# Performance work log

Measured on AMD Instinct MI355X. Metric: run time of the kernel, lower is better.

The kernel has to match this reference:

```python
import jax, jax.numpy as jnp
import numpy as np

N = 50000   # nodes
E = 1600000 # edges
K = 5       # Chebyshev order
F_IN, H1, H2, P = 32, 32, 16, 12


def setup_inputs() -> dict:
    key = jax.random.key(0)
    ks = jax.random.split(key, 16)
    x = jax.random.normal(ks[0], (N, F_IN), dtype=jnp.float32)
    edge_index = jax.random.randint(ks[1], (2, E), 0, N, dtype=jnp.int64)
    edge_weight = jax.random.uniform(ks[2], (E,), dtype=jnp.float32)
    s = 0.1
    # Cell 1: 3 gates (z, r, h), each with x-conv [K,F_IN,H1] and h-conv [K,H1,H1]
    Wx1 = jax.random.normal(ks[3], (3, K, F_IN, H1), dtype=jnp.float32) * s
    bx1 = jax.random.normal(ks[4], (3, H1), dtype=jnp.float32) * s
    Wh1 = jax.random.normal(ks[5], (3, K, H1, H1), dtype=jnp.float32) * s
    bh1 = jax.random.normal(ks[6], (3, H1), dtype=jnp.float32) * s
    # Cell 2
    Wx2 = jax.random.normal(ks[7], (3, K, H1, H2), dtype=jnp.float32) * s
    bx2 = jax.random.normal(ks[8], (3, H2), dtype=jnp.float32) * s
    Wh2 = jax.random.normal(ks[9], (3, K, H2, H2), dtype=jnp.float32) * s
    bh2 = jax.random.normal(ks[10], (3, H2), dtype=jnp.float32) * s
    # Output linear (torch convention: weight [out,in])
    Wl = jax.random.normal(ks[11], (P, H2), dtype=jnp.float32) * s
    bl = jax.random.normal(ks[12], (P,), dtype=jnp.float32) * s
    return dict(x=x, edge_index=edge_index, edge_weight=edge_weight,
                Wx1=Wx1, bx1=bx1, Wh1=Wh1, bh1=bh1,
                Wx2=Wx2, bx2=bx2, Wh2=Wh2, bh2=bh2, Wl=Wl, bl=bl)


def _cheb_norm(edge_index, edge_weight):
    # ChebConv 'sym' norm with lambda_max=2: L_hat off-diagonal = -D^-1/2 A D^-1/2,
    # diagonal cancels to 0 (get_laplacian +1 self loop, add_self_loops fill -1).
    row, col = edge_index[0], edge_index[1]
    deg = jax.ops.segment_sum(edge_weight, row, num_segments=N)
    dis = jnp.where(deg > 0, jax.lax.rsqrt(jnp.maximum(deg, 1e-30)), 0.0)
    return -dis[row] * edge_weight * dis[col]


def _gconv_gru_forward(x, edge_index, edge_weight, Wx1, bx1, Wh1, bh1,
                       Wx2, bx2, Wh2, bh2, Wl, bl):
    row, col = edge_index[0], edge_index[1]
    wn = _cheb_norm(edge_index, edge_weight)

    def spmm(v):  # (L_hat @ v): gather source rows, scatter-add to targets
        return jax.ops.segment_sum(v[row] * wn[:, None], col, num_segments=N)

    def cheb(v, W, b):  # W: [K, Fin, Fout]
        Tx0 = v
        out = Tx0 @ W[0]
        Tx1 = spmm(Tx0)
        out = out + Tx1 @ W[1]
        for k in range(2, K):
            Tx2 = 2.0 * spmm(Tx1) - Tx0
            out = out + Tx2 @ W[k]
            Tx0, Tx1 = Tx1, Tx2
        return out + b

    def gru_cell(v, H, Wx, bx, Wh, bh):
        Z = jax.nn.sigmoid(cheb(v, Wx[0], bx[0]) + cheb(H, Wh[0], bh[0]))
        R = jax.nn.sigmoid(cheb(v, Wx[1], bx[1]) + cheb(H, Wh[1], bh[1]))
        Ht = jnp.tanh(cheb(v, Wx[2], bx[2]) + cheb(H * R, Wh[2], bh[2]))
        return Z * H + (1.0 - Z) * Ht

    h = gru_cell(x, jnp.zeros((N, H1), x.dtype), Wx1, bx1, Wh1, bh1)
    h = jax.nn.relu(h)  # dropout is identity in eval mode
    h = gru_cell(h, jnp.zeros((N, H2), x.dtype), Wx2, bx2, Wh2, bh2)
    h = jax.nn.relu(h)
    return h @ Wl.T + bl


def reference(x, edge_index, edge_weight, Wx1, bx1, Wh1, bh1,
              Wx2, bx2, Wh2, bh2, Wl, bl):
    return _gconv_gru_forward(x, edge_index, edge_weight, Wx1, bx1, Wh1, bh1,
                              Wx2, bx2, Wh2, bh2, Wl, bl)
```

## Files before the change

### kernel.cpp

```cpp
#include <hip/hip_runtime.h>
#include <math.h>

#define NN 50000
#define NE 1600000
#define KORD 5
#define NB 196
#define QTR 12500
#define GE 782
#define MT 64
#define NBK 1563
#define NBP 1600
#define NCH 128
#define ECH (NE / NCH)
#define EC4 (NE / 64)
#define PADE 1800192

#define SCALE_W 2097152.0f
#define INV_SCALE_W (1.0f / 2097152.0f)
#define SCALE_D 4194304.0f
#define INV_SCALE_D (1.0f / 4194304.0f)

typedef _Float16 half8 __attribute__((ext_vector_type(8)));
typedef _Float16 half4v __attribute__((ext_vector_type(4)));
typedef float float4v __attribute__((ext_vector_type(4)));

__global__ __launch_bounds__(1024) void k_deg(const int* __restrict__ ei,
                                              const float* __restrict__ ew,
                                              int* __restrict__ deg_g) {
    __shared__ int h[QTR];
    int q = blockIdx.x >> 6, ch = blockIdx.x & 63;
    for (int i = threadIdx.x; i < QTR; i += 1024) h[i] = 0;
    __syncthreads();
    int base = ch * EC4, lo = q * QTR;
    for (int e = base + threadIdx.x; e < base + EC4; e += 1024) {
        int li = ei[e] - lo;
        if ((unsigned)li < (unsigned)QTR)
            atomicAdd(&h[li], __float2int_rn(ew[e] * SCALE_D));
    }
    __syncthreads();
    int* outp = deg_g + blockIdx.x * QTR;
    for (int i = threadIdx.x; i < QTR; i += 1024) outp[i] = h[i];
}

__global__ __launch_bounds__(256) void k_dis2(const int* __restrict__ deg_g,
                                              float* __restrict__ dis) {
    int n = blockIdx.x * 256 + threadIdx.x;
    if (n >= NN) return;
    int q = n / QTR, i = n % QTR;
    const int* p = deg_g + (q * 64) * QTR + i;
    int s = 0;
#pragma unroll
    for (int c = 0; c < 64; c++) s += p[c * QTR];
    float d = (float)s * INV_SCALE_D;
    dis[n] = s > 0 ? rsqrtf(fmaxf(d, 1e-30f)) : 0.f;
}

__global__ __launch_bounds__(1024) void k_bhist(const int* __restrict__ ei,
                                                int* __restrict__ bh) {
    __shared__ int hist[NBK];
    int ch = blockIdx.x;
    for (int i = threadIdx.x; i < NBK; i += 1024) hist[i] = 0;
    __syncthreads();
    const int* cols = ei + NE;
    int base = ch * ECH;
    for (int e = base + threadIdx.x; e < base + ECH; e += 1024)
        atomicAdd(&hist[cols[e] >> 5], 1);
    __syncthreads();
    int* outp = bh + ch * NBP;
    for (int b = threadIdx.x; b < NBK; b += 1024) outp[b] = hist[b];
}

__global__ __launch_bounds__(256) void k_btot(const int* __restrict__ bh,
                                              int* __restrict__ tot) {
    int b = blockIdx.x * 256 + threadIdx.x;
    if (b >= NBP) return;
    int s = 0;
    if (b < NBK) {
#pragma unroll 8
        for (int ch = 0; ch < NCH; ch++) s += bh[ch * NBP + b];
    }
    tot[b] = s;
}

__global__ __launch_bounds__(1024) void k_bscan1(const int* __restrict__ tot,
                                                 int* __restrict__ off_bk) {
    __shared__ int s[1024];
    int t = threadIdx.x;
    int a0 = (2 * t < NBP) ? tot[2 * t] : 0;
    int a1 = (2 * t + 1 < NBP) ? tot[2 * t + 1] : 0;
    int p0 = (a0 + 127) & ~127;
    int p1 = (a1 + 127) & ~127;
    s[t] = p0 + p1;
    __syncthreads();
    for (int d = 1; d < 1024; d <<= 1) {
        int u = (t >= d) ? s[t - d] : 0;
        __syncthreads();
        s[t] += u;
        __syncthreads();
    }
    int excl = (t == 0) ? 0 : s[t - 1];
    if (2 * t < NBK) off_bk[2 * t] = excl;
    if (2 * t + 1 < NBK) off_bk[2 * t + 1] = excl + p0;
    if (t == 1023) off_bk[NBK] = s[1023];
}

__global__ __launch_bounds__(256) void k_bcur(int* __restrict__ bh,
                                              const int* __restrict__ off_bk) {
    int b = blockIdx.x * 256 + threadIdx.x;
    if (b >= NBK) return;
    int run = off_bk[b];
    for (int ch = 0; ch < NCH; ch++) {
        int v = bh[ch * NBP + b];
        bh[ch * NBP + b] = run;
        run += v;
    }
}

__global__ __launch_bounds__(128) void k_pad(const int* __restrict__ off_bk,
                                             const int* __restrict__ tot,
                                             int2* __restrict__ edges) {
    int b = blockIdx.x;
    int start = off_bk[b] + tot[b];
    int end = off_bk[b + 1];
    for (int i = start + threadIdx.x; i < end; i += 128)
        edges[i] = make_int2(0, 0);
}

__global__ __launch_bounds__(1024) void k_cperm(const int* __restrict__ ei,
                                                const float* __restrict__ ew,
                                                const float* __restrict__ dis,
                                                const int* __restrict__ bh,
                                                int2* __restrict__ edges) {
    __shared__ int cur[NBK];
    int ch = blockIdx.x;
    const int* cp = bh + ch * NBP;
    for (int b = threadIdx.x; b < NBK; b += 1024) cur[b] = cp[b];
    __syncthreads();
    int base = ch * ECH;
    for (int e = base + threadIdx.x; e < base + ECH; e += 1024) {
        int r = ei[e], c = ei[NE + e];
        float w = -dis[r] * ew[e] * dis[c];
        int pos = atomicAdd(&cur[c >> 5], 1);
        int packed = (int)((unsigned)r | ((unsigned)(c & 31) << 16));
        edges[pos] = make_int2(packed, __float_as_int(w));
    }
}

__global__ __launch_bounds__(256) void k_spmm(const int* __restrict__ off_bk,
                                              const int2* __restrict__ edges,
                                              const float* __restrict__ vin,
                                              const float* __restrict__ prev,
                                              float* __restrict__ vout,
                                              float scale) {
    __shared__ int acc[32][33];
    int b = blockIdx.x;
    for (int i = threadIdx.x; i < 32 * 33; i += 256) (&acc[0][0])[i] = 0;
    __syncthreads();
    int e0 = off_bk[b], e1 = off_bk[b + 1];
    int group = threadIdx.x >> 3, sub = threadIdx.x & 7;
    const float4* vin4 = (const float4*)vin;
    int i = e0 + group;
    if (i < e1) {
        int2 ea = edges[i];
        int2 eb = edges[i + 32];
        int2 ec = edges[i + 64];
        int2 ed = edges[i + 96];
        while (true) {
            int ni = i + 128;
            bool more = ni < e1;
            int2 na, nb, nc, nd;
            if (more) {
                na = edges[ni];
                nb = edges[ni + 32];
                nc = edges[ni + 64];
                nd = edges[ni + 96];
            }
            unsigned ra = (unsigned)ea.x, rb = (unsigned)eb.x;
            unsigned rc = (unsigned)ec.x, rd = (unsigned)ed.x;
            float4 va = vin4[(ra & 0xffffu) * 8 + sub];
            float4 vb = vin4[(rb & 0xffffu) * 8 + sub];
            float4 vc = vin4[(rc & 0xffffu) * 8 + sub];
            float4 vd = vin4[(rd & 0xffffu) * 8 + sub];
            float wa = __int_as_float(ea.y) * SCALE_W;
            float wb = __int_as_float(eb.y) * SCALE_W;
            float wc = __int_as_float(ec.y) * SCALE_W;
            float wd = __int_as_float(ed.y) * SCALE_W;
            int* aa = &acc[ra >> 16][sub * 4];
            int* ab = &acc[rb >> 16][sub * 4];
            int* ac = &acc[rc >> 16][sub * 4];
            int* ad = &acc[rd >> 16][sub * 4];
            atomicAdd(aa + 0, __float2int_rn(wa * va.x));
            atomicAdd(aa + 1, __float2int_rn(wa * va.y));
            atomicAdd(aa + 2, __float2int_rn(wa * va.z));
            atomicAdd(aa + 3, __float2int_rn(wa * va.w));
            atomicAdd(ab + 0, __float2int_rn(wb * vb.x));
            atomicAdd(ab + 1, __float2int_rn(wb * vb.y));
            atomicAdd(ab + 2, __float2int_rn(wb * vb.z));
            atomicAdd(ab + 3, __float2int_rn(wb * vb.w));
            atomicAdd(ac + 0, __float2int_rn(wc * vc.x));
            atomicAdd(ac + 1, __float2int_rn(wc * vc.y));
            atomicAdd(ac + 2, __float2int_rn(wc * vc.z));
            atomicAdd(ac + 3, __float2int_rn(wc * vc.w));
            atomicAdd(ad + 0, __float2int_rn(wd * vd.x));
            atomicAdd(ad + 1, __float2int_rn(wd * vd.y));
            atomicAdd(ad + 2, __float2int_rn(wd * vd.z));
            atomicAdd(ad + 3, __float2int_rn(wd * vd.w));
            if (!more) break;
            i = ni; ea = na; eb = nb; ec = nc; ed = nd;
        }
    }
    __syncthreads();
    float sf = scale * INV_SCALE_W;
    int base = b << 5;
    int nl = threadIdx.x >> 3, s4 = threadIdx.x & 7;
    int n = base + nl;
    if (n < NN) {
        const int* a = &acc[nl][s4 * 4];
        float4 o;
        if (prev) {
            float4 p = ((const float4*)prev)[n * 8 + s4];
            o = make_float4(fmaf(sf, (float)a[0], -p.x),
                            fmaf(sf, (float)a[1], -p.y),
                            fmaf(sf, (float)a[2], -p.z),
                            fmaf(sf, (float)a[3], -p.w));
        } else {
            o = make_float4(sf * (float)a[0], sf * (float)a[1],
                            sf * (float)a[2], sf * (float)a[3]);
        }
        ((float4*)vout)[n * 8 + s4] = o;
    }
}

__global__ __launch_bounds__(256) void k_epi1(
    const float* __restrict__ x, const float* __restrict__ t1,
    const float* __restrict__ t2, const float* __restrict__ t3,
    const float* __restrict__ t4, const float* __restrict__ Wx1,
    const float* __restrict__ bx1, const float* __restrict__ bh1,
    float* __restrict__ h) {
    __shared__ _Float16 T[5][MT][40];
    __shared__ _Float16 Wt[64][168];
    int n0 = blockIdx.x * MT;
    const float* bufs[5] = {x, t1, t2, t3, t4};
#pragma unroll
    for (int b = 0; b < 5; b++) {
        for (int idx = threadIdx.x; idx < MT * 8; idx += 256) {
            int r = idx >> 3, c4 = idx & 7;
            int rr = n0 + r; if (rr >= NN) rr = NN - 1;
            float4 v = *(const float4*)(bufs[b] + rr * 32 + c4 * 4);
            *(half4v*)&T[b][r][c4 * 4] =
                (half4v){(_Float16)v.x, (_Float16)v.y, (_Float16)v.z, (_Float16)v.w};
        }
    }
    const float* Wz = Wx1;
    const float* Wh = Wx1 + 2 * KORD * 32 * 32;
    for (int idx = threadIdx.x; idx < 160 * 64; idx += 256) {
        int k = idx >> 6, n = idx & 63;
        int b = k >> 5, i = k & 31;
        float w = (n < 32) ? Wz[b * 1024 + i * 32 + n]
                           : Wh[b * 1024 + i * 32 + (n - 32)];
        Wt[n][k] = (_Float16)w;
    }
    __syncthreads();
    int wave = threadIdx.x >> 6;
    int lane = threadIdx.x & 63;
    int lo = lane & 15, quad = lane >> 4;
    float4v acc[4];
#pragma unroll
    for (int t = 0; t < 4; t++) acc[t] = (float4v){0.f, 0.f, 0.f, 0.f};
#pragma unroll
    for (int b = 0; b < 5; b++) {
        half8 a = *(half8*)&T[b][wave * 16 + lo][quad * 8];
#pragma unroll
        for (int t = 0; t < 4; t++) {
            half8 bf = *(half8*)&Wt[t * 16 + lo][b * 32 + quad * 8];
            acc[t] = __builtin_amdgcn_mfma_f32_16x16x32_f16(a, bf, acc[t], 0, 0, 0);
        }
    }
    int nd_base = n0 + wave * 16 + quad * 4;
#pragma unroll
    for (int t = 0; t < 2; t++) {
        int j = t * 16 + lo;
        float bz = bx1[j] + bh1[j];
        float bhb = bx1[64 + j] + bh1[64 + j];
#pragma unroll
        for (int reg = 0; reg < 4; reg++) {
            int nd = nd_base + reg;
            if (nd < NN) {
                float zz = acc[t][reg] + bz;
                float hh = acc[t + 2][reg] + bhb;
                float z = 1.f / (1.f + __expf(-zz));
                float tt = __expf(-2.f * fabsf(hh));
                float ht = copysignf((1.f - tt) / (1.f + tt), hh);
                h[nd * 32 + j] = fmaxf((1.f - z) * ht, 0.f);
            }
        }
    }
}

__global__ __launch_bounds__(256) void k_epi2(
    const float* __restrict__ hin, const float* __restrict__ t1,
    const float* __restrict__ t2, const float* __restrict__ t3,
    const float* __restrict__ t4, const float* __restrict__ Wx2,
    const float* __restrict__ bx2, const float* __restrict__ bh2,
    const float* __restrict__ Wl, const float* __restrict__ bl,
    float* __restrict__ out) {
    __shared__ _Float16 T[5][MT][40];
    __shared__ _Float16 Wt[32][168];
    __shared__ float H2[MT][17];
    int n0 = blockIdx.x * MT;
    const float* bufs[5] = {hin, t1, t2, t3, t4};
#pragma unroll
    for (int b = 0; b < 5; b++) {
        for (int idx = threadIdx.x; idx < MT * 8; idx += 256) {
            int r = idx >> 3, c4 = idx & 7;
            int rr = n0 + r; if (rr >= NN) rr = NN - 1;
            float4 v = *(const float4*)(bufs[b] + rr * 32 + c4 * 4);
            *(half4v*)&T[b][r][c4 * 4] =
                (half4v){(_Float16)v.x, (_Float16)v.y, (_Float16)v.z, (_Float16)v.w};
        }
    }
    const float* Wz = Wx2;
    const float* Wh = Wx2 + 2 * KORD * 32 * 16;
    for (int idx = threadIdx.x; idx < 160 * 32; idx += 256) {
        int k = idx >> 5, n = idx & 31;
        int b = k >> 5, i = k & 31;
        float w = (n < 16) ? Wz[b * 512 + i * 16 + n]
                           : Wh[b * 512 + i * 16 + (n - 16)];
        Wt[n][k] = (_Float16)w;
    }
    __syncthreads();
    int wave = threadIdx.x >> 6;
    int lane = threadIdx.x & 63;
    int lo = lane & 15, quad = lane >> 4;
    float4v acc[2];
    acc[0] = (float4v){0.f, 0.f, 0.f, 0.f};
    acc[1] = (float4v){0.f, 0.f, 0.f, 0.f};
#pragma unroll
    for (int b = 0; b < 5; b++) {
        half8 a = *(half8*)&T[b][wave * 16 + lo][quad * 8];
#pragma unroll
        for (int t = 0; t < 2; t++) {
            half8 bf = *(half8*)&Wt[t * 16 + lo][b * 32 + quad * 8];
            acc[t] = __builtin_amdgcn_mfma_f32_16x16x32_f16(a, bf, acc[t], 0, 0, 0);
        }
    }
    {
        int j = lo;
        float bz = bx2[j] + bh2[j];
        float bhb = bx2[32 + j] + bh2[32 + j];
        int ndl_base = wave * 16 + quad * 4;
#pragma unroll
        for (int reg = 0; reg < 4; reg++) {
            float zz = acc[0][reg] + bz;
            float hh = acc[1][reg] + bhb;
            float z = 1.f / (1.f + __expf(-zz));
            float tt = __expf(-2.f * fabsf(hh));
            float ht = copysignf((1.f - tt) / (1.f + tt), hh);
            H2[ndl_base + reg][j] = fmaxf((1.f - z) * ht, 0.f);
        }
    }
    __syncthreads();
    for (int idx = threadIdx.x; idx < MT * 12; idx += 256) {
        int n = idx / 12, p = idx % 12;
        int gn = n0 + n;
        if (gn < NN) {
            float o = bl[p];
#pragma unroll
            for (int jj = 0; jj < 16; jj++) o = fmaf(H2[n][jj], Wl[p * 16 + jj], o);
            out[gn * 12 + p] = o;
        }
    }
}


extern "C" void kernel_launch(void* const* d_in, const int* in_sizes, int n_in,
                              void* d_out, int out_size, void* d_ws, size_t ws_size,
                              hipStream_t stream) {
    const float* x   = (const float*)d_in[0];
    const int*   ei  = (const int*)d_in[1];
    const float* ew  = (const float*)d_in[2];
    const float* Wx1 = (const float*)d_in[3];
    const float* bx1 = (const float*)d_in[4];
    const float* bh1 = (const float*)d_in[6];
    const float* Wx2 = (const float*)d_in[7];
    const float* bx2 = (const float*)d_in[8];
    const float* bh2 = (const float*)d_in[10];
    const float* Wl  = (const float*)d_in[11];
    const float* bl  = (const float*)d_in[12];
    float* out = (float*)d_out;

    float* ws     = (float*)d_ws;
    float* dis    = ws;
    int*   bh     = (int*)(ws + 50048);
    int*   tot    = bh + NCH * NBP;
    int*   off_bk = tot + NBP;
    int2*  edges  = (int2*)(off_bk + NBP);
    float* T1     = (float*)(edges + PADE);
    float* T2     = T1 + NN * 32;
    float* T3     = T2 + NN * 32;
    float* T4     = T3 + NN * 32;
    float* hb     = T4 + NN * 32;
    int*   deg_g  = (int*)T1;

    k_deg  <<<256, 1024, 0, stream>>>(ei, ew, deg_g);
    k_dis2 <<<NB, 256, 0, stream>>>(deg_g, dis);
    k_bhist<<<NCH, 1024, 0, stream>>>(ei, bh);
    k_btot <<<7, 256, 0, stream>>>(bh, tot);
    k_bscan1<<<1, 1024, 0, stream>>>(tot, off_bk);
    k_bcur <<<7, 256, 0, stream>>>(bh, off_bk);
    k_pad  <<<NBK, 128, 0, stream>>>(off_bk, tot, edges);
    k_cperm<<<NCH, 1024, 0, stream>>>(ei, ew, dis, bh, edges);

    k_spmm<<<NBK, 256, 0, stream>>>(off_bk, edges, x,  nullptr, T1, 1.f);
    k_spmm<<<NBK, 256, 0, stream>>>(off_bk, edges, T1, x,       T2, 2.f);
    k_spmm<<<NBK, 256, 0, stream>>>(off_bk, edges, T2, T1,      T3, 2.f);
    k_spmm<<<NBK, 256, 0, stream>>>(off_bk, edges, T3, T2,      T4, 2.f);
    k_epi1<<<GE, 256, 0, stream>>>(x, T1, T2, T3, T4, Wx1, bx1, bh1, hb);

    k_spmm<<<NBK, 256, 0, stream>>>(off_bk, edges, hb, nullptr, T1, 1.f);
    k_spmm<<<NBK, 256, 0, stream>>>(off_bk, edges, T1, hb,      T2, 2.f);
    k_spmm<<<NBK, 256, 0, stream>>>(off_bk, edges, T2, T1,      T3, 2.f);
    k_spmm<<<NBK, 256, 0, stream>>>(off_bk, edges, T3, T2,      T4, 2.f);
    k_epi2<<<GE, 256, 0, stream>>>(hb, T1, T2, T3, T4, Wx2, bx2, bh2, Wl, bl, out);
}
```

Baseline: 376.4 us.

## Software-pipeline SpMM gathers one iteration ahead of LDS atomics; double bucketing chunks

The SpMM inner loop now issues the feature-row gathers for the current edge group and then performs the shared-memory atomic accumulation for the previous group's gathered values. This two-stage pipeline is meant to hide global gather latency behind LDS atomics. Separately, NCH doubles from 128 to 256, so the edge-bucketing kernels run with more, smaller chunks and more blocks. The pipeline holds more live registers (an extra set of float4 values), which may lower occupancy.

```diff
diff --git a/kernel.cpp b/kernel.cpp
--- a/kernel.cpp
+++ b/kernel.cpp
@@ -10,7 +10,7 @@
 #define MT 64
 #define NBK 1563
 #define NBP 1600
-#define NCH 128
+#define NCH 256
 #define ECH (NE / NCH)
 #define EC4 (NE / 64)
 #define PADE 1800192
@@ -146,6 +146,30 @@
     }
 }
 
+#define SPMM_DS(C0, W0, G0, C1, W1, G1, C2, W2, G2, C3, W3, G3)      \
+    {                                                                 \
+        int* a0 = &acc[C0][sub * 4];                                  \
+        int* a1 = &acc[C1][sub * 4];                                  \
+        int* a2 = &acc[C2][sub * 4];                                  \
+        int* a3 = &acc[C3][sub * 4];                                  \
+        atomicAdd(a0 + 0, __float2int_rn(W0 * G0.x));                 \
+        atomicAdd(a0 + 1, __float2int_rn(W0 * G0.y));                 \
+        atomicAdd(a0 + 2, __float2int_rn(W0 * G0.z));                 \
+        atomicAdd(a0 + 3, __float2int_rn(W0 * G0.w));                 \
+        atomicAdd(a1 + 0, __float2int_rn(W1 * G1.x));                 \
+        atomicAdd(a1 + 1, __float2int_rn(W1 * G1.y));                 \
+        atomicAdd(a1 + 2, __float2int_rn(W1 * G1.z));                 \
+        atomicAdd(a1 + 3, __float2int_rn(W1 * G1.w));                 \
+        atomicAdd(a2 + 0, __float2int_rn(W2 * G2.x));                 \
+        atomicAdd(a2 + 1, __float2int_rn(W2 * G2.y));                 \
+        atomicAdd(a2 + 2, __float2int_rn(W2 * G2.z));                 \
+        atomicAdd(a2 + 3, __float2int_rn(W2 * G2.w));                 \
+        atomicAdd(a3 + 0, __float2int_rn(W3 * G3.x));                 \
+        atomicAdd(a3 + 1, __float2int_rn(W3 * G3.y));                 \
+        atomicAdd(a3 + 2, __float2int_rn(W3 * G3.z));                 \
+        atomicAdd(a3 + 3, __float2int_rn(W3 * G3.w));                 \
+    }
+
 __global__ __launch_bounds__(256) void k_spmm(const int* __restrict__ off_bk,
                                               const int2* __restrict__ edges,
                                               const float* __restrict__ vin,
@@ -161,53 +185,37 @@
     const float4* vin4 = (const float4*)vin;
     int i = e0 + group;
     if (i < e1) {
-        int2 ea = edges[i];
-        int2 eb = edges[i + 32];
-        int2 ec = edges[i + 64];
-        int2 ed = edges[i + 96];
+        int2 R0 = edges[i], R1 = edges[i + 32], R2 = edges[i + 64], R3 = edges[i + 96];
+        float4 G0, G1, G2, G3;
+        int C0 = 0, C1 = 0, C2 = 0, C3 = 0;
+        float W0 = 0.f, W1 = 0.f, W2 = 0.f, W3 = 0.f;
+        bool haveG = false;
         while (true) {
             int ni = i + 128;
-            bool more = ni < e1;
-            int2 na, nb, nc, nd;
-            if (more) {
-                na = edges[ni];
-                nb = edges[ni + 32];
-                nc = edges[ni + 64];
-                nd = edges[ni + 96];
+            bool moreR = ni < e1;
+            int2 N0, N1, N2, N3;
+            if (moreR) {
+                N0 = edges[ni]; N1 = edges[ni + 32];
+                N2 = edges[ni + 64]; N3 = edges[ni + 96];
             }
-            unsigned ra = (unsigned)ea.x, rb = (unsigned)eb.x;
-            unsigned rc = (unsigned)ec.x, rd = (unsigned)ed.x;
-            float4 va = vin4[(ra & 0xffffu) * 8 + sub];
-            float4 vb = vin4[(rb & 0xffffu) * 8 + sub];
-            float4 vc = vin4[(rc & 0xffffu) * 8 + sub];
-            float4 vd = vin4[(rd & 0xffffu) * 8 + sub];
-            float wa = __int_as_float(ea.y) * SCALE_W;
-            float wb = __int_as_float(eb.y) * SCALE_W;
-            float wc = __int_as_float(ec.y) * SCALE_W;
-            float wd = __int_as_float(ed.y) * SCALE_W;
-            int* aa = &acc[ra >> 16][sub * 4];
-            int* ab = &acc[rb >> 16][sub * 4];
-            int* ac = &acc[rc >> 16][sub * 4];
-            int* ad = &acc[rd >> 16][sub * 4];
-            atomicAdd(aa + 0, __float2int_rn(wa * va.x));
-            atomicAdd(aa + 1, __float2int_rn(wa * va.y));
-            atomicAdd(aa + 2, __float2int_rn(wa * va.z));
-            atomicAdd(aa + 3, __float2int_rn(wa * va.w));
-            atomicAdd(ab + 0, __float2int_rn(wb * vb.x));
-            atomicAdd(ab + 1, __float2int_rn(wb * vb.y));
-            atomicAdd(ab + 2, __float2int_rn(wb * vb.z));
-            atomicAdd(ab + 3, __float2int_rn(wb * vb.w));
-            atomicAdd(ac + 0, __float2int_rn(wc * vc.x));
-            atomicAdd(ac + 1, __float2int_rn(wc * vc.y));
-            atomicAdd(ac + 2, __float2int_rn(wc * vc.z));
-            atomicAdd(ac + 3, __float2int_rn(wc * vc.w));
-            atomicAdd(ad + 0, __float2int_rn(wd * vd.x));
-            atomicAdd(ad + 1, __float2int_rn(wd * vd.y));
-            atomicAdd(ad + 2, __float2int_rn(wd * vd.z));
-            atomicAdd(ad + 3, __float2int_rn(wd * vd.w));
-            if (!more) break;
-            i = ni; ea = na; eb = nb; ec = nc; ed = nd;
-        }
+            float4 g0 = vin4[((unsigned)R0.x & 0xffffu) * 8 + sub];
+            float4 g1 = vin4[((unsigned)R1.x & 0xffffu) * 8 + sub];
+            float4 g2 = vin4[((unsigned)R2.x & 0xffffu) * 8 + sub];
+            float4 g3 = vin4[((unsigned)R3.x & 0xffffu) * 8 + sub];
+            if (haveG) SPMM_DS(C0, W0, G0, C1, W1, G1, C2, W2, G2, C3, W3, G3);
+            C0 = (unsigned)R0.x >> 16; C1 = (unsigned)R1.x >> 16;
+            C2 = (unsigned)R2.x >> 16; C3 = (unsigned)R3.x >> 16;
+            W0 = __int_as_float(R0.y) * SCALE_W;
+            W1 = __int_as_float(R1.y) * SCALE_W;
+            W2 = __int_as_float(R2.y) * SCALE_W;
+            W3 = __int_as_float(R3.y) * SCALE_W;
+            G0 = g0; G1 = g1; G2 = g2; G3 = g3;
+            haveG = true;
+            if (!moreR) break;
+            R0 = N0; R1 = N1; R2 = N2; R3 = N3;
+            i = ni;
+        }
+        SPMM_DS(C0, W0, G0, C1, W1, G1, C2, W2, G2, C3, W3, G3);
     }
     __syncthreads();
     float sf = scale * INV_SCALE_W;
```

Measured after the change: 364.8 us. -3.1%, faster.
